# Optimization experiments

Measured on AMD Instinct MI355X. Metric: run time of the kernel, lower is better.

## Reference

```python
import jax, jax.numpy as jnp
import numpy as np

B, F, A, U = 4096, 64, 8, 32  # batch, n_features, num_att, n_outputs
R = 2.0                       # the 'r' scaling inside exp(kernel * r)


def setup_inputs() -> dict:
    key = jax.random.key(0)
    k1, k2 = jax.random.split(key)
    inputs = jax.random.normal(k1, (B, F), dtype=jnp.float32)
    # per-exclusion-feature attention kernels, stacked: [F, A, F, U]
    limit = float(np.sqrt(6.0 / (F + U)))  # glorot_uniform
    kernels = jax.random.uniform(k2, (F, A, F, U), dtype=jnp.float32,
                                 minval=-limit, maxval=limit)
    return {"inputs": inputs, "kernels": kernels}


def reference(inputs, kernels):
    # inputs: [B, F]; kernels: [j=F excluded-feature index, A, F, U]
    f = inputs.shape[-1]
    mask = 1.0 - jnp.eye(f, dtype=inputs.dtype)          # [j, F]: zero out feature j
    xm = mask[:, None, :] * inputs[None, :, :]           # [j, B, F]
    z = jnp.einsum('jbf,jafu->jabu', xm, kernels)        # [j, A, B, U]
    z = jax.nn.softmax(z, axis=-1)                       # softmax over units
    w = jnp.exp(kernels * R)                             # [j, A, F, U]
    scores = jnp.einsum('jabu,jafu->jabf', z, w)         # [j, A, B, F]
    scores = scores.mean(axis=0)                         # mean over exclusion axis -> [A, B, F]
    return jax.nn.softmax(scores, axis=-1)               # [A, B, F]
```

## Files before the change

kernel.cpp:

```cpp
#include <hip/hip_runtime.h>
#include <hip/hip_bf16.h>
#include <math.h>

#define B_ 4096
#define F_ 64
#define A_ 8
#define U_ 32

typedef float f32x4 __attribute__((ext_vector_type(4)));
typedef short bf16x8 __attribute__((ext_vector_type(8)));

#define KD_OFF (4ull << 20)

static __device__ __forceinline__ unsigned int pk_bf16(float lo, float hi) {
    union { __hip_bfloat162 h2; unsigned int u; } cv;
    cv.h2 = __float22bfloat162_rn(make_float2(lo, hi));
    return cv.u;
}
static __device__ __forceinline__ float rb(float f) {
    unsigned int u = __float_as_uint(f);
    u += 0x7FFFu + ((u >> 16) & 1u);
    return __uint_as_float(u & 0xFFFF0000u);
}

__global__ __launch_bounds__(256) void ife_prep(const float* __restrict__ kern,
                                                unsigned char* __restrict__ ws)
{
    const int bid = blockIdx.x;
    const int a = bid >> 6, j = bid & 63;
    const int t = threadIdx.x;
    __shared__ float st[64][36];

    const float* src = kern + ((size_t)j * A_ + a) * (F_ * U_);
    {
        const int f = t >> 2, u0 = (t & 3) * 8;
        *(float4*)&st[f][u0]     = *(const float4*)&src[f * U_ + u0];
        *(float4*)&st[f][u0 + 4] = *(const float4*)&src[f * U_ + u0 + 4];
    }
    __syncthreads();

    unsigned char* dst = ws + (size_t)bid * 8192;
    const int fragid = t >> 6, lane = t & 63, q = lane >> 4, c = lane & 15;

    {
        const int kc = fragid >> 1, ut = fragid & 1;
        const int f0 = kc * 32 + q * 8, u = ut * 16 + c;
        unsigned int w[4];
        #pragma unroll
        for (int i = 0; i < 4; ++i)
            w[i] = pk_bf16(st[f0 + 2 * i][u], st[f0 + 2 * i + 1][u]);
        *(uint4*)(dst + fragid * 1024 + lane * 16) = make_uint4(w[0], w[1], w[2], w[3]);
    }
    {
        const int f = fragid * 16 + c;
        const float4 wa = *(const float4*)&st[f][q * 4];
        const float4 wb = *(const float4*)&st[f][16 + q * 4];
        unsigned int w[4];
        w[0] = pk_bf16(__expf(2.f * wa.x), __expf(2.f * wa.y));
        w[1] = pk_bf16(__expf(2.f * wa.z), __expf(2.f * wa.w));
        w[2] = pk_bf16(__expf(2.f * wb.x), __expf(2.f * wb.y));
        w[3] = pk_bf16(__expf(2.f * wb.z), __expf(2.f * wb.w));
        *(uint4*)(dst + 4096 + fragid * 1024 + lane * 16) = make_uint4(w[0], w[1], w[2], w[3]);
    }
    if (t < U_)
        ((float*)(ws + KD_OFF))[(size_t)bid * U_ + t] = rb(st[j][t]);
}

__global__ __launch_bounds__(512, 4) void ife_main(const float* __restrict__ x,
                                                   const unsigned char* __restrict__ ws,
                                                   float* __restrict__ out)
{
    const int a = blockIdx.y, bt = blockIdx.x, t = threadIdx.x;
    const int wv = t >> 6, lane = t & 63, q = lane >> 4, c = lane & 15;
    const int grp = wv >> 2, w4 = wv & 3;

    __shared__ __align__(16) float SH[6272];
    float* Xf = SH;
    float* Kd = SH + 4224;

    bf16x8 Xh[2];
    {
        const float* xr = x + (size_t)(bt * 64 + w4 * 16 + c) * F_;
        #pragma unroll
        for (int kc = 0; kc < 2; ++kc) {
            const float4 va = *(const float4*)&xr[kc * 32 + q * 8];
            const float4 vb = *(const float4*)&xr[kc * 32 + q * 8 + 4];
            union { unsigned int u[4]; bf16x8 v; } H;
            H.u[0] = pk_bf16(va.x, va.y);
            H.u[1] = pk_bf16(va.z, va.w);
            H.u[2] = pk_bf16(vb.x, vb.y);
            H.u[3] = pk_bf16(vb.z, vb.w);
            Xh[kc] = H.v;
        }
    }
    {
        const int row = t >> 3, cb = (t & 7) * 8;
        const float* xsrc = x + (size_t)(bt * 64 + row) * F_ + cb;
        const float4 v0 = *(const float4*)&xsrc[0];
        const float4 v1 = *(const float4*)&xsrc[4];
        float* xd = Xf + row * 66 + cb;
        xd[0] = rb(v0.x); xd[1] = rb(v0.y); xd[2] = rb(v0.z); xd[3] = rb(v0.w);
        xd[4] = rb(v1.x); xd[5] = rb(v1.y); xd[6] = rb(v1.z); xd[7] = rb(v1.w);
    }
    {
        const float* kd = (const float*)(ws + KD_OFF) + (size_t)a * 64 * U_;
        const int jj = t >> 3, u0 = (t & 7) * 4;
        *(float4*)&Kd[jj * 32 + u0] = *(const float4*)&kd[jj * U_ + u0];
    }
    __syncthreads();

    const unsigned char* fbase = ws + (size_t)a * 64 * 8192 + (size_t)lane * 16;
    const f32x4 vzero = (f32x4){0.f, 0.f, 0.f, 0.f};

    f32x4 S0 = vzero, S1 = vzero, S2 = vzero, S3 = vzero;

    const int jb = grp * 32;
    #pragma unroll 1
    for (int jj = 0; jj < 32; ++jj) {
        const int j = jb + jj;
        const unsigned char* p = fbase + (size_t)j * 8192;

        const bf16x8 K0 = *(const bf16x8*)(p + 0);
        const bf16x8 K1 = *(const bf16x8*)(p + 1024);
        const bf16x8 K2 = *(const bf16x8*)(p + 2048);
        const bf16x8 K3 = *(const bf16x8*)(p + 3072);
        const bf16x8 W0 = *(const bf16x8*)(p + 4096);
        const bf16x8 W1 = *(const bf16x8*)(p + 5120);
        const bf16x8 W2 = *(const bf16x8*)(p + 6144);
        const bf16x8 W3 = *(const bf16x8*)(p + 7168);

        const float xj = Xf[(w4 * 16 + c) * 66 + j];
        const f32x4 kda = *(const f32x4*)&Kd[j * 32 + q * 4];
        const f32x4 kdb = *(const f32x4*)&Kd[j * 32 + 16 + q * 4];

        f32x4 ZA = vzero, ZB = vzero;
        ZA = __builtin_amdgcn_mfma_f32_16x16x32_bf16(K0, Xh[0], ZA, 0, 0, 0);
        ZA = __builtin_amdgcn_mfma_f32_16x16x32_bf16(K2, Xh[1], ZA, 0, 0, 0);
        ZB = __builtin_amdgcn_mfma_f32_16x16x32_bf16(K1, Xh[0], ZB, 0, 0, 0);
        ZB = __builtin_amdgcn_mfma_f32_16x16x32_bf16(K3, Xh[1], ZB, 0, 0, 0);

        float eA[4], eB[4];
        #pragma unroll
        for (int r = 0; r < 4; ++r) {
            eA[r] = __expf(ZA[r] - xj * kda[r]);
            eB[r] = __expf(ZB[r] - xj * kdb[r]);
        }
        union { unsigned int u[4]; bf16x8 v; } E;
        E.u[0] = pk_bf16(eA[0], eA[1]);
        E.u[1] = pk_bf16(eA[2], eA[3]);
        E.u[2] = pk_bf16(eB[0], eB[1]);
        E.u[3] = pk_bf16(eB[2], eB[3]);

        float s = 0.f;
        #pragma unroll
        for (int i = 0; i < 4; ++i) {
            const float lo = __uint_as_float(E.u[i] << 16);
            const float hi = __uint_as_float(E.u[i] & 0xFFFF0000u);
            s += lo + hi;
        }
        s += __shfl_xor(s, 16, 64);
        s += __shfl_xor(s, 32, 64);
        const float inv = __builtin_amdgcn_rcpf(s);

        const f32x4 D0 = __builtin_amdgcn_mfma_f32_16x16x32_bf16(W0, E.v, vzero, 0, 0, 0);
        const f32x4 D1 = __builtin_amdgcn_mfma_f32_16x16x32_bf16(W1, E.v, vzero, 0, 0, 0);
        const f32x4 D2 = __builtin_amdgcn_mfma_f32_16x16x32_bf16(W2, E.v, vzero, 0, 0, 0);
        const f32x4 D3 = __builtin_amdgcn_mfma_f32_16x16x32_bf16(W3, E.v, vzero, 0, 0, 0);
        #pragma unroll
        for (int r = 0; r < 4; ++r) {
            S0[r] += D0[r] * inv;
            S1[r] += D1[r] * inv;
            S2[r] += D2[r] * inv;
            S3[r] += D3[r] * inv;
        }
    }

    __syncthreads();
    float* Sred = SH;
    if (grp == 1) {
        float* pp = Sred + (size_t)(w4 * 64 + lane) * 20;
        *(f32x4*)(pp + 0)  = S0;
        *(f32x4*)(pp + 4)  = S1;
        *(f32x4*)(pp + 8)  = S2;
        *(f32x4*)(pp + 12) = S3;
    }
    __syncthreads();
    if (grp == 0) {
        const float* pp = Sred + (size_t)(w4 * 64 + lane) * 20;
        S0 += *(const f32x4*)(pp + 0);
        S1 += *(const f32x4*)(pp + 4);
        S2 += *(const f32x4*)(pp + 8);
        S3 += *(const f32x4*)(pp + 12);

        const float sc = 1.f / 64.f;
        float ex[4][4];
        float part = 0.f;
        #pragma unroll
        for (int r = 0; r < 4; ++r) {
            ex[0][r] = __expf(S0[r] * sc);
            ex[1][r] = __expf(S1[r] * sc);
            ex[2][r] = __expf(S2[r] * sc);
            ex[3][r] = __expf(S3[r] * sc);
            part += ex[0][r] + ex[1][r] + ex[2][r] + ex[3][r];
        }
        part += __shfl_xor(part, 16, 64);
        part += __shfl_xor(part, 32, 64);
        const float inv = 1.f / part;

        const int b = bt * 64 + w4 * 16 + c;
        float* o = out + ((size_t)a * B_ + b) * F_;
        #pragma unroll
        for (int ft = 0; ft < 4; ++ft) {
            float4 v;
            v.x = ex[ft][0] * inv;
            v.y = ex[ft][1] * inv;
            v.z = ex[ft][2] * inv;
            v.w = ex[ft][3] * inv;
            *(float4*)&o[ft * 16 + q * 4] = v;
        }
    }
}

extern "C" void kernel_launch(void* const* d_in, const int* in_sizes, int n_in,
                              void* d_out, int out_size, void* d_ws, size_t ws_size,
                              hipStream_t stream) {
    (void)in_sizes; (void)n_in; (void)out_size; (void)ws_size;
    const float* x    = (const float*)d_in[0];
    const float* kern = (const float*)d_in[1];
    float* out        = (float*)d_out;
    unsigned char* ws = (unsigned char*)d_ws;

    hipLaunchKernelGGL(ife_prep, dim3(F_ * A_), dim3(256), 0, stream, kern, ws);
    hipLaunchKernelGGL(ife_main, dim3(B_ / 64, A_), dim3(512), 0, stream, x, ws, out);
}
```

Before: 99.97 us.

## Process two exclusion indices per iteration and compute softmax sums via MFMA

```diff
diff --git a/kernel.cpp b/kernel.cpp
--- a/kernel.cpp
+++ b/kernel.cpp
@@ -112,66 +112,87 @@
     const unsigned char* fbase = ws + (size_t)a * 64 * 8192 + (size_t)lane * 16;
     const f32x4 vzero = (f32x4){0.f, 0.f, 0.f, 0.f};
 
+    union { unsigned int u[4]; bf16x8 v; } oc;
+    oc.u[0] = 0x3F803F80u; oc.u[1] = 0x3F803F80u; oc.u[2] = 0x3F803F80u; oc.u[3] = 0x3F803F80u;
+    const bf16x8 ONES = oc.v;
+
     f32x4 S0 = vzero, S1 = vzero, S2 = vzero, S3 = vzero;
 
     const int jb = grp * 32;
+    const int xfrow = (w4 * 16 + c) * 66;
+
     #pragma unroll 1
-    for (int jj = 0; jj < 32; ++jj) {
-        const int j = jb + jj;
-        const unsigned char* p = fbase + (size_t)j * 8192;
-
-        const bf16x8 K0 = *(const bf16x8*)(p + 0);
-        const bf16x8 K1 = *(const bf16x8*)(p + 1024);
-        const bf16x8 K2 = *(const bf16x8*)(p + 2048);
-        const bf16x8 K3 = *(const bf16x8*)(p + 3072);
-        const bf16x8 W0 = *(const bf16x8*)(p + 4096);
-        const bf16x8 W1 = *(const bf16x8*)(p + 5120);
-        const bf16x8 W2 = *(const bf16x8*)(p + 6144);
-        const bf16x8 W3 = *(const bf16x8*)(p + 7168);
-
-        const float xj = Xf[(w4 * 16 + c) * 66 + j];
-        const f32x4 kda = *(const f32x4*)&Kd[j * 32 + q * 4];
-        const f32x4 kdb = *(const f32x4*)&Kd[j * 32 + 16 + q * 4];
-
-        f32x4 ZA = vzero, ZB = vzero;
-        ZA = __builtin_amdgcn_mfma_f32_16x16x32_bf16(K0, Xh[0], ZA, 0, 0, 0);
-        ZA = __builtin_amdgcn_mfma_f32_16x16x32_bf16(K2, Xh[1], ZA, 0, 0, 0);
-        ZB = __builtin_amdgcn_mfma_f32_16x16x32_bf16(K1, Xh[0], ZB, 0, 0, 0);
-        ZB = __builtin_amdgcn_mfma_f32_16x16x32_bf16(K3, Xh[1], ZB, 0, 0, 0);
-
-        float eA[4], eB[4];
+    for (int jj = 0; jj < 16; ++jj) {
+        const int ja = jb + jj;
+        const int jc = jb + 16 + jj;
+        const unsigned char* pa = fbase + (size_t)ja * 8192;
+        const unsigned char* pc = fbase + (size_t)jc * 8192;
+
+        const bf16x8 KA0 = *(const bf16x8*)(pa);
+        const bf16x8 KA1 = *(const bf16x8*)(pa + 1024);
+        const bf16x8 KA2 = *(const bf16x8*)(pa + 2048);
+        const bf16x8 KA3 = *(const bf16x8*)(pa + 3072);
+        const bf16x8 KC0 = *(const bf16x8*)(pc);
+        const bf16x8 KC1 = *(const bf16x8*)(pc + 1024);
+        const bf16x8 KC2 = *(const bf16x8*)(pc + 2048);
+        const bf16x8 KC3 = *(const bf16x8*)(pc + 3072);
+
+        const float xjA = Xf[xfrow + ja];
+        const float xjC = Xf[xfrow + jc];
+        const f32x4 kdaA = *(const f32x4*)&Kd[ja * 32 + q * 4];
+        const f32x4 kdbA = *(const f32x4*)&Kd[ja * 32 + 16 + q * 4];
+        const f32x4 kdaC = *(const f32x4*)&Kd[jc * 32 + q * 4];
+        const f32x4 kdbC = *(const f32x4*)&Kd[jc * 32 + 16 + q * 4];
+
+        f32x4 Z0A = vzero, Z1A = vzero, Z0C = vzero, Z1C = vzero;
+        Z0A = __builtin_amdgcn_mfma_f32_16x16x32_bf16(KA0, Xh[0], Z0A, 0, 0, 0);
+        Z0A = __builtin_amdgcn_mfma_f32_16x16x32_bf16(KA2, Xh[1], Z0A, 0, 0, 0);
+        Z1A = __builtin_amdgcn_mfma_f32_16x16x32_bf16(KA1, Xh[0], Z1A, 0, 0, 0);
+        Z1A = __builtin_amdgcn_mfma_f32_16x16x32_bf16(KA3, Xh[1], Z1A, 0, 0, 0);
+        Z0C = __builtin_amdgcn_mfma_f32_16x16x32_bf16(KC0, Xh[0], Z0C, 0, 0, 0);
+        Z0C = __builtin_amdgcn_mfma_f32_16x16x32_bf16(KC2, Xh[1], Z0C, 0, 0, 0);
+        Z1C = __builtin_amdgcn_mfma_f32_16x16x32_bf16(KC1, Xh[0], Z1C, 0, 0, 0);
+        Z1C = __builtin_amdgcn_mfma_f32_16x16x32_bf16(KC3, Xh[1], Z1C, 0, 0, 0);
+
+        const bf16x8 WA0 = *(const bf16x8*)(pa + 4096);
+        const bf16x8 WA1 = *(const bf16x8*)(pa + 5120);
+        const bf16x8 WA2 = *(const bf16x8*)(pa + 6144);
+        const bf16x8 WA3 = *(const bf16x8*)(pa + 7168);
+        const bf16x8 WC0 = *(const bf16x8*)(pc + 4096);
+        const bf16x8 WC1 = *(const bf16x8*)(pc + 5120);
+        const bf16x8 WC2 = *(const bf16x8*)(pc + 6144);
+        const bf16x8 WC3 = *(const bf16x8*)(pc + 7168);
+
+        union { unsigned int u[4]; bf16x8 v; } EA, EC;
+        EA.u[0] = pk_bf16(__expf(Z0A[0] - xjA * kdaA[0]), __expf(Z0A[1] - xjA * kdaA[1]));
+        EA.u[1] = pk_bf16(__expf(Z0A[2] - xjA * kdaA[2]), __expf(Z0A[3] - xjA * kdaA[3]));
+        EA.u[2] = pk_bf16(__expf(Z1A[0] - xjA * kdbA[0]), __expf(Z1A[1] - xjA * kdbA[1]));
+        EA.u[3] = pk_bf16(__expf(Z1A[2] - xjA * kdbA[2]), __expf(Z1A[3] - xjA * kdbA[3]));
+        EC.u[0] = pk_bf16(__expf(Z0C[0] - xjC * kdaC[0]), __expf(Z0C[1] - xjC * kdaC[1]));
+        EC.u[1] = pk_bf16(__expf(Z0C[2] - xjC * kdaC[2]), __expf(Z0C[3] - xjC * kdaC[3]));
+        EC.u[2] = pk_bf16(__expf(Z1C[0] - xjC * kdbC[0]), __expf(Z1C[1] - xjC * kdbC[1]));
+        EC.u[3] = pk_bf16(__expf(Z1C[2] - xjC * kdbC[2]), __expf(Z1C[3] - xjC * kdbC[3]));
+
+        const f32x4 svA = __builtin_amdgcn_mfma_f32_16x16x32_bf16(ONES, EA.v, vzero, 0, 0, 0);
+        const f32x4 svC = __builtin_amdgcn_mfma_f32_16x16x32_bf16(ONES, EC.v, vzero, 0, 0, 0);
+
+        const f32x4 D0A = __builtin_amdgcn_mfma_f32_16x16x32_bf16(WA0, EA.v, vzero, 0, 0, 0);
+        const f32x4 D1A = __builtin_amdgcn_mfma_f32_16x16x32_bf16(WA1, EA.v, vzero, 0, 0, 0);
+        const f32x4 D2A = __builtin_amdgcn_mfma_f32_16x16x32_bf16(WA2, EA.v, vzero, 0, 0, 0);
+        const f32x4 D3A = __builtin_amdgcn_mfma_f32_16x16x32_bf16(WA3, EA.v, vzero, 0, 0, 0);
+        const f32x4 D0C = __builtin_amdgcn_mfma_f32_16x16x32_bf16(WC0, EC.v, vzero, 0, 0, 0);
+        const f32x4 D1C = __builtin_amdgcn_mfma_f32_16x16x32_bf16(WC1, EC.v, vzero, 0, 0, 0);
+        const f32x4 D2C = __builtin_amdgcn_mfma_f32_16x16x32_bf16(WC2, EC.v, vzero, 0, 0, 0);
+        const f32x4 D3C = __builtin_amdgcn_mfma_f32_16x16x32_bf16(WC3, EC.v, vzero, 0, 0, 0);
+
+        const float invA = __builtin_amdgcn_rcpf(svA[0]);
+        const float invC = __builtin_amdgcn_rcpf(svC[0]);
         #pragma unroll
         for (int r = 0; r < 4; ++r) {
-            eA[r] = __expf(ZA[r] - xj * kda[r]);
-            eB[r] = __expf(ZB[r] - xj * kdb[r]);
-        }
-        union { unsigned int u[4]; bf16x8 v; } E;
-        E.u[0] = pk_bf16(eA[0], eA[1]);
-        E.u[1] = pk_bf16(eA[2], eA[3]);
-        E.u[2] = pk_bf16(eB[0], eB[1]);
-        E.u[3] = pk_bf16(eB[2], eB[3]);
-
-        float s = 0.f;
-        #pragma unroll
-        for (int i = 0; i < 4; ++i) {
-            const float lo = __uint_as_float(E.u[i] << 16);
-            const float hi = __uint_as_float(E.u[i] & 0xFFFF0000u);
-            s += lo + hi;
-        }
-        s += __shfl_xor(s, 16, 64);
-        s += __shfl_xor(s, 32, 64);
-        const float inv = __builtin_amdgcn_rcpf(s);
-
-        const f32x4 D0 = __builtin_amdgcn_mfma_f32_16x16x32_bf16(W0, E.v, vzero, 0, 0, 0);
-        const f32x4 D1 = __builtin_amdgcn_mfma_f32_16x16x32_bf16(W1, E.v, vzero, 0, 0, 0);
-        const f32x4 D2 = __builtin_amdgcn_mfma_f32_16x16x32_bf16(W2, E.v, vzero, 0, 0, 0);
-        const f32x4 D3 = __builtin_amdgcn_mfma_f32_16x16x32_bf16(W3, E.v, vzero, 0, 0, 0);
-        #pragma unroll
-        for (int r = 0; r < 4; ++r) {
-            S0[r] += D0[r] * inv;
-            S1[r] += D1[r] * inv;
-            S2[r] += D2[r] * inv;
-            S3[r] += D3[r] * inv;
+            S0[r] += D0A[r] * invA; S0[r] += D0C[r] * invC;
+            S1[r] += D1A[r] * invA; S1[r] += D1C[r] * invC;
+            S2[r] += D2A[r] * invA; S2[r] += D2C[r] * invC;
+            S3[r] += D3A[r] * invA; S3[r] += D3C[r] * invC;
         }
     }
 
```

Measured after the change: 99.35 us. No clear change (-0.6%).

## Double-buffer kernel fragments in LDS via async global_load_lds and MFMA row-sum

Applied to the files above, without the earlier changes.

```diff
diff --git a/kernel.cpp b/kernel.cpp
--- a/kernel.cpp
+++ b/kernel.cpp
@@ -75,6 +75,7 @@
     const int grp = wv >> 2, w4 = wv & 3;
 
     __shared__ __align__(16) float SH[6272];
+    __shared__ __align__(16) unsigned char Fbuf[2][2][8192];
     float* Xf = SH;
     float* Kd = SH + 4224;
 
@@ -107,29 +108,47 @@
         const int jj = t >> 3, u0 = (t & 7) * 4;
         *(float4*)&Kd[jj * 32 + u0] = *(const float4*)&kd[jj * U_ + u0];
     }
+
+    const unsigned char* blob = ws + (size_t)a * 64 * 8192;
+    const f32x4 vzero = (f32x4){0.f, 0.f, 0.f, 0.f};
+
+    union { unsigned int u[4]; bf16x8 v; } oc;
+    oc.u[0] = 0x3F803F80u; oc.u[1] = 0x3F803F80u; oc.u[2] = 0x3F803F80u; oc.u[3] = 0x3F803F80u;
+    const bf16x8 ONES = oc.v;
+
+    f32x4 S0 = vzero, S1 = vzero, S2 = vzero, S3 = vzero;
+
+    typedef const __attribute__((address_space(1))) unsigned int gau32;
+    typedef __attribute__((address_space(3))) unsigned int lau32;
+    auto STAGE = [&](int buf, int s) {
+        const int tg = wv >> 2, fp = wv & 3;
+        const int jt = tg * 32 + s;
+        const unsigned char* g = blob + (size_t)jt * 8192 + fp * 2048 + lane * 16;
+        unsigned char* l = &Fbuf[buf][tg][fp * 2048];
+        __builtin_amdgcn_global_load_lds((gau32*)(g),        (lau32*)(l),        16, 0, 0);
+        __builtin_amdgcn_global_load_lds((gau32*)(g + 1024), (lau32*)(l + 1024), 16, 0, 0);
+    };
+
+    const int jb = grp * 32;
+    const int xfrow = (w4 * 16 + c) * 66;
+
+    STAGE(0, 0);
     __syncthreads();
 
-    const unsigned char* fbase = ws + (size_t)a * 64 * 8192 + (size_t)lane * 16;
-    const f32x4 vzero = (f32x4){0.f, 0.f, 0.f, 0.f};
-
-    f32x4 S0 = vzero, S1 = vzero, S2 = vzero, S3 = vzero;
-
-    const int jb = grp * 32;
+    int cur = 0;
     #pragma unroll 1
-    for (int jj = 0; jj < 32; ++jj) {
-        const int j = jb + jj;
-        const unsigned char* p = fbase + (size_t)j * 8192;
-
-        const bf16x8 K0 = *(const bf16x8*)(p + 0);
-        const bf16x8 K1 = *(const bf16x8*)(p + 1024);
-        const bf16x8 K2 = *(const bf16x8*)(p + 2048);
-        const bf16x8 K3 = *(const bf16x8*)(p + 3072);
-        const bf16x8 W0 = *(const bf16x8*)(p + 4096);
-        const bf16x8 W1 = *(const bf16x8*)(p + 5120);
-        const bf16x8 W2 = *(const bf16x8*)(p + 6144);
-        const bf16x8 W3 = *(const bf16x8*)(p + 7168);
-
-        const float xj = Xf[(w4 * 16 + c) * 66 + j];
+    for (int s = 0; s < 32; ++s) {
+        if (s < 31) STAGE(cur ^ 1, s + 1);
+
+        const unsigned char* pt = &Fbuf[cur][grp][lane * 16];
+        const int j = jb + s;
+
+        const bf16x8 K0 = *(const bf16x8*)(pt);
+        const bf16x8 K1 = *(const bf16x8*)(pt + 1024);
+        const bf16x8 K2 = *(const bf16x8*)(pt + 2048);
+        const bf16x8 K3 = *(const bf16x8*)(pt + 3072);
+
+        const float xj = Xf[xfrow + j];
         const f32x4 kda = *(const f32x4*)&Kd[j * 32 + q * 4];
         const f32x4 kdb = *(const f32x4*)&Kd[j * 32 + 16 + q * 4];
 
@@ -139,33 +158,25 @@
         ZB = __builtin_amdgcn_mfma_f32_16x16x32_bf16(K1, Xh[0], ZB, 0, 0, 0);
         ZB = __builtin_amdgcn_mfma_f32_16x16x32_bf16(K3, Xh[1], ZB, 0, 0, 0);
 
-        float eA[4], eB[4];
-        #pragma unroll
-        for (int r = 0; r < 4; ++r) {
-            eA[r] = __expf(ZA[r] - xj * kda[r]);
-            eB[r] = __expf(ZB[r] - xj * kdb[r]);
-        }
+        const bf16x8 W0 = *(const bf16x8*)(pt + 4096);
+        const bf16x8 W1 = *(const bf16x8*)(pt + 5120);
+        const bf16x8 W2 = *(const bf16x8*)(pt + 6144);
+        const bf16x8 W3 = *(const bf16x8*)(pt + 7168);
+
         union { unsigned int u[4]; bf16x8 v; } E;
-        E.u[0] = pk_bf16(eA[0], eA[1]);
-        E.u[1] = pk_bf16(eA[2], eA[3]);
-        E.u[2] = pk_bf16(eB[0], eB[1]);
-        E.u[3] = pk_bf16(eB[2], eB[3]);
-
-        float s = 0.f;
-        #pragma unroll
-        for (int i = 0; i < 4; ++i) {
-            const float lo = __uint_as_float(E.u[i] << 16);
-            const float hi = __uint_as_float(E.u[i] & 0xFFFF0000u);
-            s += lo + hi;
-        }
-        s += __shfl_xor(s, 16, 64);
-        s += __shfl_xor(s, 32, 64);
-        const float inv = __builtin_amdgcn_rcpf(s);
+        E.u[0] = pk_bf16(__expf(ZA[0] - xj * kda[0]), __expf(ZA[1] - xj * kda[1]));
+        E.u[1] = pk_bf16(__expf(ZA[2] - xj * kda[2]), __expf(ZA[3] - xj * kda[3]));
+        E.u[2] = pk_bf16(__expf(ZB[0] - xj * kdb[0]), __expf(ZB[1] - xj * kdb[1]));
+        E.u[3] = pk_bf16(__expf(ZB[2] - xj * kdb[2]), __expf(ZB[3] - xj * kdb[3]));
+
+        const f32x4 sv = __builtin_amdgcn_mfma_f32_16x16x32_bf16(ONES, E.v, vzero, 0, 0, 0);
 
         const f32x4 D0 = __builtin_amdgcn_mfma_f32_16x16x32_bf16(W0, E.v, vzero, 0, 0, 0);
         const f32x4 D1 = __builtin_amdgcn_mfma_f32_16x16x32_bf16(W1, E.v, vzero, 0, 0, 0);
         const f32x4 D2 = __builtin_amdgcn_mfma_f32_16x16x32_bf16(W2, E.v, vzero, 0, 0, 0);
         const f32x4 D3 = __builtin_amdgcn_mfma_f32_16x16x32_bf16(W3, E.v, vzero, 0, 0, 0);
+
+        const float inv = __builtin_amdgcn_rcpf(sv[0]);
         #pragma unroll
         for (int r = 0; r < 4; ++r) {
             S0[r] += D0[r] * inv;
@@ -173,9 +184,11 @@
             S2[r] += D2[r] * inv;
             S3[r] += D3[r] * inv;
         }
-    }
-
-    __syncthreads();
+
+        __syncthreads();
+        cur ^= 1;
+    }
+
     float* Sred = SH;
     if (grp == 1) {
         float* pp = Sred + (size_t)(w4 * 64 + lane) * 20;
```

Result: faster. 96.16 us (-3.8%).

## Fold diagonal mask and log2e into kernel frags; compute softmax sums via MFMA

Applied to the files above, without the earlier changes.

```diff
diff --git a/kernel.cpp b/kernel.cpp
--- a/kernel.cpp
+++ b/kernel.cpp
@@ -10,17 +10,11 @@
 typedef float f32x4 __attribute__((ext_vector_type(4)));
 typedef short bf16x8 __attribute__((ext_vector_type(8)));
 
-#define KD_OFF (4ull << 20)
 
 static __device__ __forceinline__ unsigned int pk_bf16(float lo, float hi) {
     union { __hip_bfloat162 h2; unsigned int u; } cv;
     cv.h2 = __float22bfloat162_rn(make_float2(lo, hi));
     return cv.u;
-}
-static __device__ __forceinline__ float rb(float f) {
-    unsigned int u = __float_as_uint(f);
-    u += 0x7FFFu + ((u >> 16) & 1u);
-    return __uint_as_float(u & 0xFFFF0000u);
 }
 
 __global__ __launch_bounds__(256) void ife_prep(const float* __restrict__ kern,
@@ -41,14 +35,19 @@
 
     unsigned char* dst = ws + (size_t)bid * 8192;
     const int fragid = t >> 6, lane = t & 63, q = lane >> 4, c = lane & 15;
+    const float L2E = 1.44269504088896341f;
 
     {
         const int kc = fragid >> 1, ut = fragid & 1;
         const int f0 = kc * 32 + q * 8, u = ut * 16 + c;
         unsigned int w[4];
         #pragma unroll
-        for (int i = 0; i < 4; ++i)
-            w[i] = pk_bf16(st[f0 + 2 * i][u], st[f0 + 2 * i + 1][u]);
+        for (int i = 0; i < 4; ++i) {
+            const int fA = f0 + 2 * i, fB = f0 + 2 * i + 1;
+            const float vA = (fA == j) ? 0.f : st[fA][u] * L2E;
+            const float vB = (fB == j) ? 0.f : st[fB][u] * L2E;
+            w[i] = pk_bf16(vA, vB);
+        }
         *(uint4*)(dst + fragid * 1024 + lane * 16) = make_uint4(w[0], w[1], w[2], w[3]);
     }
     {
@@ -62,8 +61,6 @@
         w[3] = pk_bf16(__expf(2.f * wb.z), __expf(2.f * wb.w));
         *(uint4*)(dst + 4096 + fragid * 1024 + lane * 16) = make_uint4(w[0], w[1], w[2], w[3]);
     }
-    if (t < U_)
-        ((float*)(ws + KD_OFF))[(size_t)bid * U_ + t] = rb(st[j][t]);
 }
 
 __global__ __launch_bounds__(512, 4) void ife_main(const float* __restrict__ x,
@@ -74,9 +71,7 @@
     const int wv = t >> 6, lane = t & 63, q = lane >> 4, c = lane & 15;
     const int grp = wv >> 2, w4 = wv & 3;
 
-    __shared__ __align__(16) float SH[6272];
-    float* Xf = SH;
-    float* Kd = SH + 4224;
+    __shared__ __align__(16) float SH[5120];
 
     bf16x8 Xh[2];
     {
@@ -93,34 +88,22 @@
             Xh[kc] = H.v;
         }
     }
-    {
-        const int row = t >> 3, cb = (t & 7) * 8;
-        const float* xsrc = x + (size_t)(bt * 64 + row) * F_ + cb;
-        const float4 v0 = *(const float4*)&xsrc[0];
-        const float4 v1 = *(const float4*)&xsrc[4];
-        float* xd = Xf + row * 66 + cb;
-        xd[0] = rb(v0.x); xd[1] = rb(v0.y); xd[2] = rb(v0.z); xd[3] = rb(v0.w);
-        xd[4] = rb(v1.x); xd[5] = rb(v1.y); xd[6] = rb(v1.z); xd[7] = rb(v1.w);
-    }
-    {
-        const float* kd = (const float*)(ws + KD_OFF) + (size_t)a * 64 * U_;
-        const int jj = t >> 3, u0 = (t & 7) * 4;
-        *(float4*)&Kd[jj * 32 + u0] = *(const float4*)&kd[jj * U_ + u0];
-    }
-    __syncthreads();
 
     const unsigned char* fbase = ws + (size_t)a * 64 * 8192 + (size_t)lane * 16;
     const f32x4 vzero = (f32x4){0.f, 0.f, 0.f, 0.f};
+
+    union { unsigned int u[4]; bf16x8 v; } oc;
+    oc.u[0] = 0x3F803F80u; oc.u[1] = 0x3F803F80u; oc.u[2] = 0x3F803F80u; oc.u[3] = 0x3F803F80u;
+    const bf16x8 ONES = oc.v;
 
     f32x4 S0 = vzero, S1 = vzero, S2 = vzero, S3 = vzero;
 
     const int jb = grp * 32;
     #pragma unroll 1
     for (int jj = 0; jj < 32; ++jj) {
-        const int j = jb + jj;
-        const unsigned char* p = fbase + (size_t)j * 8192;
-
-        const bf16x8 K0 = *(const bf16x8*)(p + 0);
+        const unsigned char* p = fbase + (size_t)(jb + jj) * 8192;
+
+        const bf16x8 K0 = *(const bf16x8*)(p);
         const bf16x8 K1 = *(const bf16x8*)(p + 1024);
         const bf16x8 K2 = *(const bf16x8*)(p + 2048);
         const bf16x8 K3 = *(const bf16x8*)(p + 3072);
@@ -129,43 +112,26 @@
         const bf16x8 W2 = *(const bf16x8*)(p + 6144);
         const bf16x8 W3 = *(const bf16x8*)(p + 7168);
 
-        const float xj = Xf[(w4 * 16 + c) * 66 + j];
-        const f32x4 kda = *(const f32x4*)&Kd[j * 32 + q * 4];
-        const f32x4 kdb = *(const f32x4*)&Kd[j * 32 + 16 + q * 4];
-
         f32x4 ZA = vzero, ZB = vzero;
         ZA = __builtin_amdgcn_mfma_f32_16x16x32_bf16(K0, Xh[0], ZA, 0, 0, 0);
         ZA = __builtin_amdgcn_mfma_f32_16x16x32_bf16(K2, Xh[1], ZA, 0, 0, 0);
         ZB = __builtin_amdgcn_mfma_f32_16x16x32_bf16(K1, Xh[0], ZB, 0, 0, 0);
         ZB = __builtin_amdgcn_mfma_f32_16x16x32_bf16(K3, Xh[1], ZB, 0, 0, 0);
 
-        float eA[4], eB[4];
-        #pragma unroll
-        for (int r = 0; r < 4; ++r) {
-            eA[r] = __expf(ZA[r] - xj * kda[r]);
-            eB[r] = __expf(ZB[r] - xj * kdb[r]);
-        }
         union { unsigned int u[4]; bf16x8 v; } E;
-        E.u[0] = pk_bf16(eA[0], eA[1]);
-        E.u[1] = pk_bf16(eA[2], eA[3]);
-        E.u[2] = pk_bf16(eB[0], eB[1]);
-        E.u[3] = pk_bf16(eB[2], eB[3]);
-
-        float s = 0.f;
-        #pragma unroll
-        for (int i = 0; i < 4; ++i) {
-            const float lo = __uint_as_float(E.u[i] << 16);
-            const float hi = __uint_as_float(E.u[i] & 0xFFFF0000u);
-            s += lo + hi;
-        }
-        s += __shfl_xor(s, 16, 64);
-        s += __shfl_xor(s, 32, 64);
-        const float inv = __builtin_amdgcn_rcpf(s);
+        E.u[0] = pk_bf16(exp2f(ZA[0]), exp2f(ZA[1]));
+        E.u[1] = pk_bf16(exp2f(ZA[2]), exp2f(ZA[3]));
+        E.u[2] = pk_bf16(exp2f(ZB[0]), exp2f(ZB[1]));
+        E.u[3] = pk_bf16(exp2f(ZB[2]), exp2f(ZB[3]));
+
+        const f32x4 sv = __builtin_amdgcn_mfma_f32_16x16x32_bf16(ONES, E.v, vzero, 0, 0, 0);
 
         const f32x4 D0 = __builtin_amdgcn_mfma_f32_16x16x32_bf16(W0, E.v, vzero, 0, 0, 0);
         const f32x4 D1 = __builtin_amdgcn_mfma_f32_16x16x32_bf16(W1, E.v, vzero, 0, 0, 0);
         const f32x4 D2 = __builtin_amdgcn_mfma_f32_16x16x32_bf16(W2, E.v, vzero, 0, 0, 0);
         const f32x4 D3 = __builtin_amdgcn_mfma_f32_16x16x32_bf16(W3, E.v, vzero, 0, 0, 0);
+
+        const float inv = __builtin_amdgcn_rcpf(sv[0]);
         #pragma unroll
         for (int r = 0; r < 4; ++r) {
             S0[r] += D0[r] * inv;
@@ -192,15 +158,15 @@
         S2 += *(const f32x4*)(pp + 8);
         S3 += *(const f32x4*)(pp + 12);
 
-        const float sc = 1.f / 64.f;
+        const float sc2 = 1.44269504088896341f / 64.f;
         float ex[4][4];
         float part = 0.f;
         #pragma unroll
         for (int r = 0; r < 4; ++r) {
-            ex[0][r] = __expf(S0[r] * sc);
-            ex[1][r] = __expf(S1[r] * sc);
-            ex[2][r] = __expf(S2[r] * sc);
-            ex[3][r] = __expf(S3[r] * sc);
+            ex[0][r] = exp2f(S0[r] * sc2);
+            ex[1][r] = exp2f(S1[r] * sc2);
+            ex[2][r] = exp2f(S2[r] * sc2);
+            ex[3][r] = exp2f(S3[r] * sc2);
             part += ex[0][r] + ex[1][r] + ex[2][r] + ex[3][r];
         }
         part += __shfl_xor(part, 16, 64);
```

After: 101.4 us. Within noise of the previous version (+1.4%).
